# Kernel optimization log

Hardware: AMD Instinct MI355X
Metric: run time of the kernel (lower is better)

## Reference

```python
import jax, jax.numpy as jnp
import numpy as np

EPS = 1e-6
K = 20
NUM_OBJECTS = 50
OBJ_FEAT = 256
C_DIM = 128
HIDDEN = 128


def vn_linear(x, W):
    # x: [B, C, 3, ...]; W: [O, C] -> [B, O, 3, ...]
    return jnp.einsum('oc,bc...->bo...', W, x)


def vn_leaky(x, Wdir, slope):
    d = vn_linear(x, Wdir)
    dot = jnp.sum(x * d, axis=2, keepdims=True)
    dsq = jnp.sum(d * d, axis=2, keepdims=True)
    x_neg = x - (dot / (dsq + EPS)) * d
    return slope * x + (1.0 - slope) * jnp.where(dot >= 0, x, x_neg)


def vn_linear_leaky(x, Wfeat, Wdir, slope):
    pf = vn_linear(x, Wfeat)
    d = vn_linear(x, Wdir)
    dot = jnp.sum(pf * d, axis=2, keepdims=True)
    dsq = jnp.sum(d * d, axis=2, keepdims=True)
    p_neg = pf - (dot / (dsq + EPS)) * d
    return slope * pf + (1.0 - slope) * jnp.where(dot >= 0, pf, p_neg)


def resblock(x, fc0, fc1, a0, a1, sc):
    net = vn_linear(vn_leaky(x, a0, 0.0), fc0)
    dx = vn_linear(vn_leaky(net, a1, 0.0), fc1)
    return vn_linear(x, sc) + dx


def get_graph_feature_cross(x, k):
    # x: [B, 3, N] -> edge features [B, 3, 3, N, k]
    inner = -2.0 * jnp.einsum('bdn,bdm->bnm', x, x)
    xx = jnp.sum(x * x, axis=1)                       # [B, N]
    neg_dist = -xx[:, :, None] - inner - xx[:, None, :]  # [B, N, N]
    idx = jax.lax.top_k(neg_dist, k)[1]               # [B, N, k] nearest neighbors
    xt = jnp.transpose(x, (0, 2, 1))                  # [B, N, 3]
    nbr = jax.vmap(lambda pts, ind: pts[ind])(xt, idx)  # [B, N, k, 3]
    ctr = jnp.broadcast_to(xt[:, :, None, :], nbr.shape)
    cross = jnp.cross(nbr, ctr)
    feat = jnp.stack([nbr - ctr, ctr, cross], axis=3)  # [B, N, k, 3, 3]
    return jnp.transpose(feat, (0, 3, 4, 1, 2))


def mlp2(zf, w0, w1, w2):
    h = jax.nn.relu(zf @ w0.T)
    h = jax.nn.relu(h @ w1.T)
    return h @ w2.T


def setup_inputs():
    key = jax.random.key(0)
    ks = jax.random.split(key, 24)
    B, N = 4, 4096

    def rn(k, shape):
        return jax.random.normal(k, shape, dtype=jnp.float32) * (1.0 / np.sqrt(shape[-1]))

    return {
        'p': jax.random.normal(ks[0], (B, N, 3), dtype=jnp.float32),
        'z_idxs': jax.random.randint(ks[1], (B,), 0, NUM_OBJECTS),
        'z': jax.random.normal(ks[2], (NUM_OBJECTS, OBJ_FEAT), dtype=jnp.float32),
        'hw0': rn(ks[3], (OBJ_FEAT, OBJ_FEAT)),
        'hw1': rn(ks[4], (OBJ_FEAT, OBJ_FEAT)),
        'hw2': rn(ks[5], (C_DIM * HIDDEN, OBJ_FEAT)),
        'hb0': rn(ks[6], (OBJ_FEAT, OBJ_FEAT)),
        'hb1': rn(ks[7], (OBJ_FEAT, OBJ_FEAT)),
        'hb2': rn(ks[8], (C_DIM, OBJ_FEAT)),
        'conv_pos_feat': rn(ks[9], (128, 3)),
        'conv_pos_dir': rn(ks[10], (128, 3)),
        'fc_pos_w': rn(ks[11], (2 * HIDDEN, 128)),
        'blk_fc0': rn(ks[12], (5, HIDDEN, 2 * HIDDEN)),
        'blk_fc1': rn(ks[13], (5, HIDDEN, HIDDEN)),
        'blk_act0': rn(ks[14], (5, 2 * HIDDEN, 2 * HIDDEN)),
        'blk_act1': rn(ks[15], (5, HIDDEN, HIDDEN)),
        'blk_sc': rn(ks[16], (5, HIDDEN, 2 * HIDDEN)),
        'actc_dir': rn(ks[17], (HIDDEN, HIDDEN)),
    }


def reference(p, z_idxs, z, hw0, hw1, hw2, hb0, hb1, hb2, conv_pos_feat,
              conv_pos_dir, fc_pos_w, blk_fc0, blk_fc1, blk_act0, blk_act1,
              blk_sc, actc_dir):
    B = p.shape[0]
    x = jnp.transpose(p, (0, 2, 1))                       # [B, 3, N]
    feat = get_graph_feature_cross(x, K)                  # [B, 3, 3, N, k]
    net = vn_linear_leaky(feat, conv_pos_feat, conv_pos_dir, 0.2)  # [B,128,3,N,k]
    net = jnp.mean(net, axis=-1)                          # [B,128,3,N]
    net = vn_linear(net, fc_pos_w)                        # [B,256,3,N]
    for i in range(5):
        net = resblock(net, blk_fc0[i], blk_fc1[i], blk_act0[i], blk_act1[i], blk_sc[i])
        if i < 4:
            pooled = jnp.mean(net, axis=-1, keepdims=True)
            net = jnp.concatenate([net, jnp.broadcast_to(pooled, net.shape)], axis=1)
    net = vn_leaky(jnp.mean(net, axis=-1), actc_dir, 0.2)  # [B, HIDDEN, 3]
    zf = z[z_idxs]                                        # [B, OBJ_FEAT]
    w = mlp2(zf, hw0, hw1, hw2).reshape(B, C_DIM, HIDDEN)  # hypernet weights
    b = mlp2(zf, hb0, hb1, hb2)                           # [B, C_DIM]
    c = jnp.einsum('bhd,bch->bcd', net, w) + b[:, :, None]  # [B, C_DIM, 3]
    return c
```

## Files before the change

kernel.cpp:

```cpp
#include <hip/hip_runtime.h>
#include <hip/hip_fp16.h>
#include <cstdint>
#include <cstddef>

#define NPTS 4096
#define BATCH 4
#define KNN 20

typedef __half f16;
using f32x4 = __attribute__((ext_vector_type(4))) float;
using f16x8 = __attribute__((ext_vector_type(8))) _Float16;

__global__ __launch_bounds__(256) void knn_kernel(const float* __restrict__ p,
                                                  int* __restrict__ idx_out) {
    __shared__ float pts[12288];
    const int tid  = threadIdx.x;
    const int wave = tid >> 6, lane = tid & 63;
    const int b  = blockIdx.x >> 10;
    const int nb = ((blockIdx.x & 1023) << 2) + wave;

    const float4* src4 = (const float4*)(p + (size_t)b * NPTS * 3);
    float4* dst4 = (float4*)pts;
    for (int i = tid; i < NPTS * 3 / 4; i += 256) dst4[i] = src4[i];
    __syncthreads();

    const float cx = pts[3 * nb], cy = pts[3 * nb + 1], cz = pts[3 * nb + 2];
    unsigned lst[4];
#pragma unroll
    for (int i = 0; i < 4; i++) lst[i] = 0xFFFFFFFFu;

    for (int t = 0; t < NPTS / 64; t++) {
        int m = (t << 6) + lane;
        float dx = pts[3 * m] - cx, dy = pts[3 * m + 1] - cy, dz = pts[3 * m + 2] - cz;
        float d = dx * dx + dy * dy + dz * dz;
        unsigned c = (__float_as_uint(d) & 0xFFFFF000u) | (unsigned)m;
#pragma unroll
        for (int j = 0; j < 4; j++) {
            unsigned lo = min(c, lst[j]);
            c = max(c, lst[j]);
            lst[j] = lo;
        }
    }

    unsigned lo = 0u, hi = 0xFFFFFFFFu;
    for (int it = 0; it < 32; it++) {
        unsigned mid = lo + ((hi - lo) >> 1);
        int cnt = __popcll(__ballot(lst[0] <= mid)) + __popcll(__ballot(lst[1] <= mid))
                + __popcll(__ballot(lst[2] <= mid)) + __popcll(__ballot(lst[3] <= mid));
        if (cnt >= KNN) hi = mid; else lo = mid + 1;
    }
    const unsigned T = hi;

    unsigned long long bl[4];
#pragma unroll
    for (int j = 0; j < 4; j++) bl[j] = __ballot(lst[j] <= T);
    const unsigned long long lmask = (lane == 63) ? ~0ull >> 1 : (1ull << lane) - 1;
    int base = 0;
    const size_t out_base = ((size_t)b * NPTS + nb) * KNN;
#pragma unroll
    for (int j = 0; j < 4; j++) {
        if (lst[j] <= T) {
            int pos = base + (int)__popcll(bl[j] & lmask);
            idx_out[out_base + pos] = (int)(lst[j] & 0xFFFu);
        }
        base += (int)__popcll(bl[j]);
    }
}

__global__ __launch_bounds__(128) void edgeconv_kernel(
    const float* __restrict__ p, const int* __restrict__ idx,
    const float* __restrict__ wf, const float* __restrict__ wd,
    f16* __restrict__ out) {
    __shared__ float e[KNN][6];
    const int col = blockIdx.x;
    const int b = col >> 12;
    const int tid = threadIdx.x;
    const float cx = p[(size_t)col * 3], cy = p[(size_t)col * 3 + 1], cz = p[(size_t)col * 3 + 2];
    if (tid < KNN) {
        int j = idx[(size_t)col * KNN + tid];
        const float* q = &p[((size_t)b * NPTS + j) * 3];
        float nx = q[0], ny = q[1], nz = q[2];
        e[tid][0] = nx - cx; e[tid][1] = ny - cy; e[tid][2] = nz - cz;
        e[tid][3] = ny * cz - nz * cy;
        e[tid][4] = nz * cx - nx * cz;
        e[tid][5] = nx * cy - ny * cx;
    }
    __syncthreads();
    const int o = tid;
    const float f0 = wf[o * 3], f1 = wf[o * 3 + 1], f2 = wf[o * 3 + 2];
    const float g0 = wd[o * 3], g1 = wd[o * 3 + 1], g2 = wd[o * 3 + 2];
    const float pc0 = f1 * cx, pc1 = f1 * cy, pc2 = f1 * cz;
    const float gc0 = g1 * cx, gc1 = g1 * cy, gc2 = g1 * cz;
    float a0 = 0.f, a1 = 0.f, a2 = 0.f;
    for (int k = 0; k < KNN; k++) {
        float d0 = e[k][0], d1 = e[k][1], d2 = e[k][2];
        float c0 = e[k][3], c1 = e[k][4], c2 = e[k][5];
        float pf0 = fmaf(f0, d0, fmaf(f2, c0, pc0));
        float pf1 = fmaf(f0, d1, fmaf(f2, c1, pc1));
        float pf2 = fmaf(f0, d2, fmaf(f2, c2, pc2));
        float dd0 = fmaf(g0, d0, fmaf(g2, c0, gc0));
        float dd1 = fmaf(g0, d1, fmaf(g2, c1, gc1));
        float dd2 = fmaf(g0, d2, fmaf(g2, c2, gc2));
        float dot = pf0 * dd0 + pf1 * dd1 + pf2 * dd2;
        float dsq = dd0 * dd0 + dd1 * dd1 + dd2 * dd2;
        float w = 0.8f * dot * __builtin_amdgcn_rcpf(dsq + 1e-6f);
        w = (dot >= 0.f) ? 0.f : w;
        a0 += pf0 - w * dd0;
        a1 += pf1 - w * dd1;
        a2 += pf2 - w * dd2;
    }
    const float inv = 1.f / (float)KNN;
    out[((size_t)col * 3 + 0) * 128 + o] = __float2half(a0 * inv);
    out[((size_t)col * 3 + 1) * 128 + o] = __float2half(a1 * inv);
    out[((size_t)col * 3 + 2) * 128 + o] = __float2half(a2 * inv);
}

template <int KIN>
__global__ __launch_bounds__(256) void resblock_kernel(
    const uint16_t* __restrict__ INg,
    const uint16_t* __restrict__ Wfcp,
    const uint16_t* __restrict__ Wa0,
    const uint16_t* __restrict__ Wfc0,
    const uint16_t* __restrict__ Wa1,
    const uint16_t* __restrict__ Wsc,
    const uint16_t* __restrict__ Wfc1,
    const float* __restrict__ PBg,
    const float* __restrict__ BAg,
    const float* __restrict__ BSCg,
    f16* __restrict__ OUTg,
    float* __restrict__ PPg) {
    constexpr int XRB  = (KIN == 256) ? 528 : 272;
    constexpr int INS_OFF = (KIN == 256) ? 13056 : 0;
    constexpr int H0_OFF  = (KIN == 256) ? 38400 : 14592;
    constexpr int MID_OFF = (KIN == 256) ? 0 : 27648;
    constexpr int LDS_SZ  = (KIN == 256) ? 51456 : 40704;
    __shared__ char lds[LDS_SZ];
    char* MBs = lds;
    char* INs = lds + INS_OFF;
    float* PBs = (float*)(lds + 13056);
    char* H0h = lds + H0_OFF;
    char* MID = lds + MID_OFF;

    const int tid = threadIdx.x;
    const int lane = tid & 63;
    const int wc = tid >> 6;
    const int gr0 = blockIdx.x * 48;
    const int b = blockIdx.x >> 8;

    if (KIN == 128) {
        for (int i = tid; i < 384; i += 256) PBs[i] = PBg[b * 384 + i];
    }
    {
        char* dst = (KIN == 256) ? MBs : INs;
#pragma unroll
        for (int j = 0; j < 3; j++) {
            int chunk = tid + j * 256;
            int row = chunk >> 4, c16 = chunk & 15;
            f16x8 v = *(const f16x8*)(INg + (size_t)(gr0 + row) * 128 + c16 * 8);
            *(f16x8*)(dst + row * 272 + c16 * 16) = v;
        }
    }
    __syncthreads();

    if (KIN == 256) {
        f32x4 acc[3][4];
#pragma unroll
        for (int i = 0; i < 3; i++)
#pragma unroll
            for (int j = 0; j < 4; j++) acc[i][j] = (f32x4){0.f, 0.f, 0.f, 0.f};
#pragma unroll
        for (int ks = 0; ks < 4; ks++) {
            const int kb = ks * 64 + (lane >> 4) * 16;
            f16x8 af[3], bf[4];
#pragma unroll
            for (int mi = 0; mi < 3; mi++) {
                int r = mi * 16 + (lane & 15);
                af[mi] = *(const f16x8*)(MBs + r * 272 + kb);
            }
#pragma unroll
            for (int ni = 0; ni < 4; ni++) {
                int o = wc * 64 + ni * 16 + (lane & 15);
                bf[ni] = *(const f16x8*)(Wfcp + o * 128 + ks * 32 + (lane >> 4) * 8);
            }
#pragma unroll
            for (int mi = 0; mi < 3; mi++)
#pragma unroll
                for (int ni = 0; ni < 4; ni++)
                    acc[mi][ni] = __builtin_amdgcn_mfma_f32_16x16x32_f16(
                        af[mi], bf[ni], acc[mi][ni], 0, 0, 0);
        }
#pragma unroll
        for (int mi = 0; mi < 3; mi++)
#pragma unroll
            for (int ni = 0; ni < 4; ni++) {
                int col = wc * 64 + ni * 16 + (lane & 15);
#pragma unroll
                for (int r = 0; r < 4; r++) {
                    int row = mi * 16 + (lane >> 4) * 4 + r;
                    *(f16*)(INs + row * XRB + col * 2) = __float2half(acc[mi][ni][r]);
                }
            }
        __syncthreads();
    }

    f32x4 midAcc[3][2];
#pragma unroll
    for (int i = 0; i < 3; i++) { midAcc[i][0] = (f32x4){0,0,0,0}; midAcc[i][1] = (f32x4){0,0,0,0}; }

#pragma unroll
    for (int half = 0; half < 2; half++) {
        {
            f32x4 acc[3][2];
#pragma unroll
            for (int i = 0; i < 3; i++) { acc[i][0] = (f32x4){0,0,0,0}; acc[i][1] = (f32x4){0,0,0,0}; }
#pragma unroll
            for (int ks = 0; ks < KIN / 32; ks++) {
                const int kb = ks * 64 + (lane >> 4) * 16;
                f16x8 af[3], bf[2];
#pragma unroll
                for (int mi = 0; mi < 3; mi++) {
                    int r = mi * 16 + (lane & 15);
                    af[mi] = *(const f16x8*)(INs + r * XRB + kb);
                }
#pragma unroll
                for (int ni = 0; ni < 2; ni++) {
                    int o = half * 128 + wc * 32 + ni * 16 + (lane & 15);
                    bf[ni] = *(const f16x8*)(Wa0 + o * 256 + ks * 32 + (lane >> 4) * 8);
                }
#pragma unroll
                for (int mi = 0; mi < 3; mi++)
#pragma unroll
                    for (int ni = 0; ni < 2; ni++)
                        acc[mi][ni] = __builtin_amdgcn_mfma_f32_16x16x32_f16(
                            af[mi], bf[ni], acc[mi][ni], 0, 0, 0);
            }
#pragma unroll
            for (int mi = 0; mi < 3; mi++)
#pragma unroll
                for (int ni = 0; ni < 2; ni++) {
                    int col = wc * 32 + ni * 16 + (lane & 15);
#pragma unroll
                    for (int r = 0; r < 4; r++) {
                        int row = mi * 16 + (lane >> 4) * 4 + r;
                        float v = acc[mi][ni][r];
                        if (KIN == 128)
                            v += BAg[b * 768 + (row % 3) * 256 + half * 128 + col];
                        *(f16*)(H0h + row * 272 + col * 2) = __float2half(v);
                    }
                }
        }
        __syncthreads();
#pragma unroll
        for (int j = 0; j < 4; j++) {
            int it = tid + j * 256;
            int pnt = it >> 6, cp = it & 63;
            float xv[3][2], dv[3][2];
#pragma unroll
            for (int s = 0; s < 3; s++) {
                int row = pnt * 3 + s;
                __half2 d2 = *(const __half2*)(H0h + row * 272 + cp * 4);
                dv[s][0] = __half2float(d2.x); dv[s][1] = __half2float(d2.y);
                if (KIN == 256) {
                    __half2 x2 = *(const __half2*)(INs + row * XRB + half * 256 + cp * 4);
                    xv[s][0] = __half2float(x2.x); xv[s][1] = __half2float(x2.y);
                } else {
                    if (half == 0) {
                        __half2 x2 = *(const __half2*)(INs + row * XRB + cp * 4);
                        xv[s][0] = __half2float(x2.x); xv[s][1] = __half2float(x2.y);
                    } else {
                        xv[s][0] = PBs[s * 128 + cp * 2];
                        xv[s][1] = PBs[s * 128 + cp * 2 + 1];
                    }
                }
            }
#pragma unroll
            for (int jj = 0; jj < 2; jj++) {
                float dot = xv[0][jj] * dv[0][jj] + xv[1][jj] * dv[1][jj] + xv[2][jj] * dv[2][jj];
                float dsq = dv[0][jj] * dv[0][jj] + dv[1][jj] * dv[1][jj] + dv[2][jj] * dv[2][jj];
                float coef = dot * __builtin_amdgcn_rcpf(dsq + 1e-6f);
                bool pos = dot >= 0.f;
#pragma unroll
                for (int s = 0; s < 3; s++)
                    xv[s][jj] = pos ? xv[s][jj] : xv[s][jj] - coef * dv[s][jj];
            }
#pragma unroll
            for (int s = 0; s < 3; s++) {
                int row = pnt * 3 + s;
                __half2 h2;
                h2.x = __float2half(xv[s][0]);
                h2.y = __float2half(xv[s][1]);
                *(__half2*)(H0h + row * 272 + cp * 4) = h2;
            }
        }
        __syncthreads();
#pragma unroll
        for (int ks = 0; ks < 4; ks++) {
            const int kb = ks * 64 + (lane >> 4) * 16;
            f16x8 af[3], bf[2];
#pragma unroll
            for (int mi = 0; mi < 3; mi++) {
                int r = mi * 16 + (lane & 15);
                af[mi] = *(const f16x8*)(H0h + r * 272 + kb);
            }
#pragma unroll
            for (int ni = 0; ni < 2; ni++) {
                int o = wc * 32 + ni * 16 + (lane & 15);
                bf[ni] = *(const f16x8*)(Wfc0 + o * 256 + half * 128 + ks * 32 + (lane >> 4) * 8);
            }
#pragma unroll
            for (int mi = 0; mi < 3; mi++)
#pragma unroll
                for (int ni = 0; ni < 2; ni++)
                    midAcc[mi][ni] = __builtin_amdgcn_mfma_f32_16x16x32_f16(
                        af[mi], bf[ni], midAcc[mi][ni], 0, 0, 0);
        }
        __syncthreads();
    }

#pragma unroll
    for (int mi = 0; mi < 3; mi++)
#pragma unroll
        for (int ni = 0; ni < 2; ni++) {
            int col = wc * 32 + ni * 16 + (lane & 15);
#pragma unroll
            for (int r = 0; r < 4; r++) {
                int row = mi * 16 + (lane >> 4) * 4 + r;
                *(f16*)(MID + row * 272 + col * 2) = __float2half(midAcc[mi][ni][r]);
            }
        }
    __syncthreads();

    {
        f32x4 acc[3][2];
#pragma unroll
        for (int i = 0; i < 3; i++) { acc[i][0] = (f32x4){0,0,0,0}; acc[i][1] = (f32x4){0,0,0,0}; }
#pragma unroll
        for (int ks = 0; ks < 4; ks++) {
            const int kb = ks * 64 + (lane >> 4) * 16;
            f16x8 af[3], bf[2];
#pragma unroll
            for (int mi = 0; mi < 3; mi++) {
                int r = mi * 16 + (lane & 15);
                af[mi] = *(const f16x8*)(MID + r * 272 + kb);
            }
#pragma unroll
            for (int ni = 0; ni < 2; ni++) {
                int o = wc * 32 + ni * 16 + (lane & 15);
                bf[ni] = *(const f16x8*)(Wa1 + o * 128 + ks * 32 + (lane >> 4) * 8);
            }
#pragma unroll
            for (int mi = 0; mi < 3; mi++)
#pragma unroll
                for (int ni = 0; ni < 2; ni++)
                    acc[mi][ni] = __builtin_amdgcn_mfma_f32_16x16x32_f16(
                        af[mi], bf[ni], acc[mi][ni], 0, 0, 0);
        }
#pragma unroll
        for (int mi = 0; mi < 3; mi++)
#pragma unroll
            for (int ni = 0; ni < 2; ni++) {
                int col = wc * 32 + ni * 16 + (lane & 15);
#pragma unroll
                for (int r = 0; r < 4; r++) {
                    int row = mi * 16 + (lane >> 4) * 4 + r;
                    *(f16*)(H0h + row * 272 + col * 2) = __float2half(acc[mi][ni][r]);
                }
            }
    }
    __syncthreads();
#pragma unroll
    for (int j = 0; j < 4; j++) {
        int it = tid + j * 256;
        int pnt = it >> 6, cp = it & 63;
        float xv[3][2], dv[3][2];
#pragma unroll
        for (int s = 0; s < 3; s++) {
            int row = pnt * 3 + s;
            __half2 d2 = *(const __half2*)(H0h + row * 272 + cp * 4);
            __half2 x2 = *(const __half2*)(MID + row * 272 + cp * 4);
            dv[s][0] = __half2float(d2.x); dv[s][1] = __half2float(d2.y);
            xv[s][0] = __half2float(x2.x); xv[s][1] = __half2float(x2.y);
        }
#pragma unroll
        for (int jj = 0; jj < 2; jj++) {
            float dot = xv[0][jj] * dv[0][jj] + xv[1][jj] * dv[1][jj] + xv[2][jj] * dv[2][jj];
            float dsq = dv[0][jj] * dv[0][jj] + dv[1][jj] * dv[1][jj] + dv[2][jj] * dv[2][jj];
            float coef = dot * __builtin_amdgcn_rcpf(dsq + 1e-6f);
            bool pos = dot >= 0.f;
#pragma unroll
            for (int s = 0; s < 3; s++)
                xv[s][jj] = pos ? xv[s][jj] : xv[s][jj] - coef * dv[s][jj];
        }
#pragma unroll
        for (int s = 0; s < 3; s++) {
            int row = pnt * 3 + s;
            __half2 h2;
            h2.x = __float2half(xv[s][0]);
            h2.y = __float2half(xv[s][1]);
            *(__half2*)(H0h + row * 272 + cp * 4) = h2;
        }
    }
    __syncthreads();

    {
        f32x4 acc[3][2];
#pragma unroll
        for (int i = 0; i < 3; i++) { acc[i][0] = (f32x4){0,0,0,0}; acc[i][1] = (f32x4){0,0,0,0}; }
        constexpr int NKS = (KIN + 128) / 32;
#pragma unroll
        for (int ks = 0; ks < NKS; ks++) {
            const int kelem = ks * 32;
            f16x8 af[3], bf[2];
            if (kelem < KIN) {
                const int kb = kelem * 2 + (lane >> 4) * 16;
#pragma unroll
                for (int mi = 0; mi < 3; mi++) {
                    int r = mi * 16 + (lane & 15);
                    af[mi] = *(const f16x8*)(INs + r * XRB + kb);
                }
#pragma unroll
                for (int ni = 0; ni < 2; ni++) {
                    int o = wc * 32 + ni * 16 + (lane & 15);
                    bf[ni] = *(const f16x8*)(Wsc + o * 256 + kelem + (lane >> 4) * 8);
                }
            } else {
                const int kk = kelem - KIN;
                const int kb = kk * 2 + (lane >> 4) * 16;
#pragma unroll
                for (int mi = 0; mi < 3; mi++) {
                    int r = mi * 16 + (lane & 15);
                    af[mi] = *(const f16x8*)(H0h + r * 272 + kb);
                }
#pragma unroll
                for (int ni = 0; ni < 2; ni++) {
                    int o = wc * 32 + ni * 16 + (lane & 15);
                    bf[ni] = *(const f16x8*)(Wfc1 + o * 128 + kk + (lane >> 4) * 8);
                }
            }
#pragma unroll
            for (int mi = 0; mi < 3; mi++)
#pragma unroll
                for (int ni = 0; ni < 2; ni++)
                    acc[mi][ni] = __builtin_amdgcn_mfma_f32_16x16x32_f16(
                        af[mi], bf[ni], acc[mi][ni], 0, 0, 0);
        }
        float ps[2][3] = {};
#pragma unroll
        for (int mi = 0; mi < 3; mi++)
#pragma unroll
            for (int ni = 0; ni < 2; ni++) {
                int col = wc * 32 + ni * 16 + (lane & 15);
#pragma unroll
                for (int r = 0; r < 4; r++) {
                    int row = mi * 16 + (lane >> 4) * 4 + r;
                    float v = acc[mi][ni][r];
                    if (KIN == 128) v += BSCg[b * 384 + (row % 3) * 128 + col];
                    OUTg[(size_t)(gr0 + row) * 128 + col] = __float2half(v);
                    ps[ni][row % 3] += v;
                }
            }
#pragma unroll
        for (int ni = 0; ni < 2; ni++)
#pragma unroll
            for (int s = 0; s < 3; s++) {
                float x = ps[ni][s];
                x += __shfl_xor(x, 16, 64);
                x += __shfl_xor(x, 32, 64);
                ps[ni][s] = x;
            }
        if ((lane >> 4) == 0) {
#pragma unroll
            for (int ni = 0; ni < 2; ni++) {
                int col = wc * 32 + ni * 16 + (lane & 15);
#pragma unroll
                for (int s = 0; s < 3; s++)
                    PPg[(size_t)blockIdx.x * 384 + s * 128 + col] = ps[ni][s];
            }
        }
    }
}

__global__ __launch_bounds__(512) void poolbias_kernel(
    const float* __restrict__ PP, const f16* __restrict__ a0n, const f16* __restrict__ scn,
    float* __restrict__ PB, float* __restrict__ BA, float* __restrict__ BSC, int hasbias) {
    __shared__ float red[4][128];
    __shared__ float pl[128];
    const int bs = blockIdx.x;
    const int b = bs / 3, s = bs % 3;
    const int t = threadIdx.x;
    const int col = t & 127, seg = t >> 7;
    {
        float acc = 0.f;
        const float* base = PP + (size_t)(b * 256) * 384 + s * 128 + col;
        for (int k = seg * 64; k < seg * 64 + 64; k++) acc += base[(size_t)k * 384];
        red[seg][col] = acc;
    }
    __syncthreads();
    if (t < 128) {
        float a = (red[0][t] + red[1][t]) + (red[2][t] + red[3][t]);
        a *= (1.f / (float)NPTS);
        pl[t] = a;
        PB[bs * 128 + t] = a;
    }
    __syncthreads();
    if (!hasbias) return;
    if (t < 256) {
        float s2 = 0.f;
        for (int c = 0; c < 128; c++) s2 += __half2float(a0n[t * 256 + 128 + c]) * pl[c];
        BA[bs * 256 + t] = s2;
    } else if (t < 384) {
        int o = t - 256;
        float s2 = 0.f;
        for (int c = 0; c < 128; c++) s2 += __half2float(scn[o * 256 + 128 + c]) * pl[c];
        BSC[bs * 128 + o] = s2;
    }
}

__global__ void cvt_all(const float* __restrict__ fcpw, const float* __restrict__ act0,
                        const float* __restrict__ fc0, const float* __restrict__ act1,
                        const float* __restrict__ fc1, const float* __restrict__ scw,
                        f16* o_fcpw, f16* o_act0, f16* o_fc0, f16* o_act1, f16* o_fc1,
                        f16* o_scw) {
    int i = blockIdx.x * 256 + threadIdx.x;
    if (i < 32768) { o_fcpw[i] = __float2half(fcpw[i]); }
    else if (i < 360448) { int j = i - 32768;  o_act0[j] = __float2half(act0[j]); }
    else if (i < 524288) { int j = i - 360448; o_fc0[j]  = __float2half(fc0[j]); }
    else if (i < 606208) { int j = i - 524288; o_act1[j] = __float2half(act1[j]); }
    else if (i < 688128) { int j = i - 606208; o_fc1[j]  = __float2half(fc1[j]); }
    else                 { int j = i - 688128; o_scw[j]  = __float2half(scw[j]); }
}

__global__ __launch_bounds__(256) void hypermlp_kernel(
    const float* __restrict__ z, const int* __restrict__ zidx,
    const float* __restrict__ hw0, const float* __restrict__ hw1,
    const float* __restrict__ hb0, const float* __restrict__ hb1,
    const float* __restrict__ hb2,
    float* __restrict__ H2, float* __restrict__ BV) {
    __shared__ float zf[256], ta[256], tb[256];
    const int b = blockIdx.x, o = threadIdx.x;
    zf[o] = z[(size_t)zidx[b] * 256 + o];
    __syncthreads();
    float s = 0.f;
    for (int c = 0; c < 256; c++) s += zf[c] * hw0[o * 256 + c];
    ta[o] = fmaxf(s, 0.f);
    __syncthreads();
    s = 0.f;
    for (int c = 0; c < 256; c++) s += ta[c] * hw1[o * 256 + c];
    tb[o] = fmaxf(s, 0.f);
    __syncthreads();
    H2[(size_t)b * 256 + o] = tb[o];
    s = 0.f;
    for (int c = 0; c < 256; c++) s += zf[c] * hb0[o * 256 + c];
    __syncthreads();
    ta[o] = fmaxf(s, 0.f);
    __syncthreads();
    s = 0.f;
    for (int c = 0; c < 256; c++) s += ta[c] * hb1[o * 256 + c];
    __syncthreads();
    tb[o] = fmaxf(s, 0.f);
    __syncthreads();
    if (o < 128) {
        s = 0.f;
        for (int c = 0; c < 256; c++) s += tb[c] * hb2[o * 256 + c];
        BV[(size_t)b * 128 + o] = s;
    }
}

__global__ __launch_bounds__(256) void wmat_kernel(const float* __restrict__ H2,
                                                   const float* __restrict__ hw2,
                                                   float* __restrict__ WM) {
    __shared__ float h[256];
    const int b = blockIdx.y;
    const int row = blockIdx.x * 256 + threadIdx.x;
    h[threadIdx.x] = H2[(size_t)b * 256 + threadIdx.x];
    __syncthreads();
    float s = 0.f;
    for (int c = 0; c < 256; c++) s += h[c] * hw2[(size_t)row * 256 + c];
    WM[(size_t)b * 16384 + row] = s;
}

__global__ __launch_bounds__(384) void final_out_kernel(
    const float* __restrict__ pb, const float* __restrict__ actc,
    const float* __restrict__ WM, const float* __restrict__ BV,
    float* __restrict__ out) {
    __shared__ float pb2s[3][128];
    const int b = blockIdx.x;
    const int t = threadIdx.x;
    if (t < 128) {
        const int o = t;
        float d0 = 0.f, d1 = 0.f, d2 = 0.f;
        for (int c = 0; c < 128; c++) {
            float w = actc[o * 128 + c];
            d0 += w * pb[(size_t)(b * 3 + 0) * 128 + c];
            d1 += w * pb[(size_t)(b * 3 + 1) * 128 + c];
            d2 += w * pb[(size_t)(b * 3 + 2) * 128 + c];
        }
        float x0 = pb[(size_t)(b * 3 + 0) * 128 + o];
        float x1 = pb[(size_t)(b * 3 + 1) * 128 + o];
        float x2 = pb[(size_t)(b * 3 + 2) * 128 + o];
        float dot = x0 * d0 + x1 * d1 + x2 * d2;
        float dsq = d0 * d0 + d1 * d1 + d2 * d2;
        float coef = dot / (dsq + 1e-6f);
        bool pos = dot >= 0.f;
        float h0 = pos ? x0 : x0 - coef * d0;
        float h1 = pos ? x1 : x1 - coef * d1;
        float h2 = pos ? x2 : x2 - coef * d2;
        pb2s[0][o] = 0.2f * x0 + 0.8f * h0;
        pb2s[1][o] = 0.2f * x1 + 0.8f * h1;
        pb2s[2][o] = 0.2f * x2 + 0.8f * h2;
    }
    __syncthreads();
    const int cd = t / 3, d = t % 3;
    float s = BV[(size_t)b * 128 + cd];
    for (int h = 0; h < 128; h++)
        s += pb2s[d][h] * WM[(size_t)b * 16384 + cd * 128 + h];
    out[(size_t)b * 384 + cd * 3 + d] = s;
}

extern "C" void kernel_launch(void* const* d_in, const int* in_sizes, int n_in,
                              void* d_out, int out_size, void* d_ws, size_t ws_size,
                              hipStream_t stream) {
    (void)in_sizes; (void)n_in; (void)out_size; (void)ws_size;
    const float* p     = (const float*)d_in[0];
    const int*   zidx  = (const int*)d_in[1];
    const float* z     = (const float*)d_in[2];
    const float* hw0   = (const float*)d_in[3];
    const float* hw1   = (const float*)d_in[4];
    const float* hw2   = (const float*)d_in[5];
    const float* hb0   = (const float*)d_in[6];
    const float* hb1   = (const float*)d_in[7];
    const float* hb2   = (const float*)d_in[8];
    const float* cpf   = (const float*)d_in[9];
    const float* cpd   = (const float*)d_in[10];
    const float* fcpw  = (const float*)d_in[11];
    const float* fc0w  = (const float*)d_in[12];
    const float* fc1w  = (const float*)d_in[13];
    const float* act0  = (const float*)d_in[14];
    const float* act1  = (const float*)d_in[15];
    const float* scw   = (const float*)d_in[16];
    const float* actc  = (const float*)d_in[17];
    float* out = (float*)d_out;
    char* ws = (char*)d_ws;

    int*   IDX   = (int*)(ws + 0);
    f16*   MB    = (f16*)(ws + 1310720);
    f16*   MB2   = (f16*)(ws + 13893632);
    f16*   FCPW16= (f16*)(ws + 26476544);
    f16*   ACT0W = (f16*)(ws + 26542080);
    f16*   FC0W  = (f16*)(ws + 27197440);
    f16*   ACT1W = (f16*)(ws + 27525120);
    f16*   FC1W  = (f16*)(ws + 27688960);
    f16*   SCW16 = (f16*)(ws + 27852800);
    float* PP    = (float*)(ws + 28180480);
    float* PB    = (float*)(ws + 29753344);
    float* H2    = (float*)(ws + 29759488);
    float* BV    = (float*)(ws + 29763584);
    float* WM    = (float*)(ws + 29765632);
    float* BA    = (float*)(ws + 30027776);
    float* BSC   = (float*)(ws + 30040064);

    cvt_all<<<3328, 256, 0, stream>>>(fcpw, act0, fc0w, act1, fc1w, scw,
                                      FCPW16, ACT0W, FC0W, ACT1W, FC1W, SCW16);

    knn_kernel<<<BATCH * NPTS / 4, 256, 0, stream>>>(p, IDX);
    edgeconv_kernel<<<BATCH * NPTS, 128, 0, stream>>>(p, IDX, cpf, cpd, MB);

    resblock_kernel<256><<<1024, 256, 0, stream>>>(
        (const uint16_t*)MB, (const uint16_t*)FCPW16,
        (const uint16_t*)ACT0W, (const uint16_t*)FC0W,
        (const uint16_t*)ACT1W, (const uint16_t*)SCW16, (const uint16_t*)FC1W,
        nullptr, nullptr, nullptr, MB2, PP);
    poolbias_kernel<<<12, 512, 0, stream>>>(PP, ACT0W + 1 * 65536, SCW16 + 1 * 32768,
                                            PB, BA, BSC, 1);

    for (int i = 1; i < 5; i++) {
        const f16* a0h = ACT0W + (size_t)i * 256 * 256;
        const f16* sch = SCW16 + (size_t)i * 128 * 256;
        f16* in  = (i & 1) ? MB2 : MB;
        f16* ob  = (i & 1) ? MB : MB2;
        resblock_kernel<128><<<1024, 256, 0, stream>>>(
            (const uint16_t*)in, nullptr,
            (const uint16_t*)a0h,
            (const uint16_t*)(FC0W + (size_t)i * 128 * 256),
            (const uint16_t*)(ACT1W + (size_t)i * 128 * 128),
            (const uint16_t*)sch,
            (const uint16_t*)(FC1W + (size_t)i * 128 * 128),
            PB, BA, BSC, ob, PP);
        if (i < 4) {
            poolbias_kernel<<<12, 512, 0, stream>>>(
                PP, ACT0W + (size_t)(i + 1) * 65536, SCW16 + (size_t)(i + 1) * 32768,
                PB, BA, BSC, 1);
        } else {
            poolbias_kernel<<<12, 512, 0, stream>>>(PP, nullptr, nullptr, PB, BA, BSC, 0);
        }
    }

    hypermlp_kernel<<<4, 256, 0, stream>>>(z, zidx, hw0, hw1, hb0, hb1, hb2, H2, BV);
    wmat_kernel<<<dim3(64, 4), 256, 0, stream>>>(H2, hw2, WM);
    final_out_kernel<<<4, 384, 0, stream>>>(PB, actc, WM, BV, out);
}
```

Baseline: 394.4 us.

## Double resblock workgroup to 512 threads, each wave computing 16 output columns

```diff
diff --git a/kernel.cpp b/kernel.cpp
--- a/kernel.cpp
+++ b/kernel.cpp
@@ -116,7 +116,7 @@
 }
 
 template <int KIN>
-__global__ __launch_bounds__(256) void resblock_kernel(
+__global__ __launch_bounds__(512) void resblock_kernel(
     const uint16_t* __restrict__ INg,
     const uint16_t* __restrict__ Wfcp,
     const uint16_t* __restrict__ Wa0,
@@ -148,13 +148,11 @@
     const int b = blockIdx.x >> 8;
 
     if (KIN == 128) {
-        for (int i = tid; i < 384; i += 256) PBs[i] = PBg[b * 384 + i];
+        if (tid < 384) PBs[tid] = PBg[b * 384 + tid];
     }
     {
         char* dst = (KIN == 256) ? MBs : INs;
-#pragma unroll
-        for (int j = 0; j < 3; j++) {
-            int chunk = tid + j * 256;
+        for (int chunk = tid; chunk < 768; chunk += 512) {
             int row = chunk >> 4, c16 = chunk & 15;
             f16x8 v = *(const f16x8*)(INg + (size_t)(gr0 + row) * 128 + c16 * 8);
             *(f16x8*)(dst + row * 272 + c16 * 16) = v;
@@ -163,37 +161,35 @@
     __syncthreads();
 
     if (KIN == 256) {
-        f32x4 acc[3][4];
-#pragma unroll
-        for (int i = 0; i < 3; i++)
-#pragma unroll
-            for (int j = 0; j < 4; j++) acc[i][j] = (f32x4){0.f, 0.f, 0.f, 0.f};
+        f32x4 acc[3][2];
+#pragma unroll
+        for (int i = 0; i < 3; i++) { acc[i][0] = (f32x4){0,0,0,0}; acc[i][1] = (f32x4){0,0,0,0}; }
 #pragma unroll
         for (int ks = 0; ks < 4; ks++) {
             const int kb = ks * 64 + (lane >> 4) * 16;
-            f16x8 af[3], bf[4];
+            f16x8 af[3], bf[2];
 #pragma unroll
             for (int mi = 0; mi < 3; mi++) {
                 int r = mi * 16 + (lane & 15);
                 af[mi] = *(const f16x8*)(MBs + r * 272 + kb);
             }
 #pragma unroll
-            for (int ni = 0; ni < 4; ni++) {
-                int o = wc * 64 + ni * 16 + (lane & 15);
+            for (int ni = 0; ni < 2; ni++) {
+                int o = wc * 32 + ni * 16 + (lane & 15);
                 bf[ni] = *(const f16x8*)(Wfcp + o * 128 + ks * 32 + (lane >> 4) * 8);
             }
 #pragma unroll
             for (int mi = 0; mi < 3; mi++)
 #pragma unroll
-                for (int ni = 0; ni < 4; ni++)
+                for (int ni = 0; ni < 2; ni++)
                     acc[mi][ni] = __builtin_amdgcn_mfma_f32_16x16x32_f16(
                         af[mi], bf[ni], acc[mi][ni], 0, 0, 0);
         }
 #pragma unroll
         for (int mi = 0; mi < 3; mi++)
 #pragma unroll
-            for (int ni = 0; ni < 4; ni++) {
-                int col = wc * 64 + ni * 16 + (lane & 15);
+            for (int ni = 0; ni < 2; ni++) {
+                int col = wc * 32 + ni * 16 + (lane & 15);
 #pragma unroll
                 for (int r = 0; r < 4; r++) {
                     int row = mi * 16 + (lane >> 4) * 4 + r;
@@ -203,56 +199,51 @@
         __syncthreads();
     }
 
-    f32x4 midAcc[3][2];
-#pragma unroll
-    for (int i = 0; i < 3; i++) { midAcc[i][0] = (f32x4){0,0,0,0}; midAcc[i][1] = (f32x4){0,0,0,0}; }
+    f32x4 midAcc[3];
+#pragma unroll
+    for (int i = 0; i < 3; i++) midAcc[i] = (f32x4){0, 0, 0, 0};
 
 #pragma unroll
     for (int half = 0; half < 2; half++) {
         {
-            f32x4 acc[3][2];
-#pragma unroll
-            for (int i = 0; i < 3; i++) { acc[i][0] = (f32x4){0,0,0,0}; acc[i][1] = (f32x4){0,0,0,0}; }
+            f32x4 acc[3];
+#pragma unroll
+            for (int i = 0; i < 3; i++) acc[i] = (f32x4){0, 0, 0, 0};
 #pragma unroll
             for (int ks = 0; ks < KIN / 32; ks++) {
                 const int kb = ks * 64 + (lane >> 4) * 16;
-                f16x8 af[3], bf[2];
+                f16x8 af[3], bf;
 #pragma unroll
                 for (int mi = 0; mi < 3; mi++) {
                     int r = mi * 16 + (lane & 15);
                     af[mi] = *(const f16x8*)(INs + r * XRB + kb);
                 }
-#pragma unroll
-                for (int ni = 0; ni < 2; ni++) {
-                    int o = half * 128 + wc * 32 + ni * 16 + (lane & 15);
-                    bf[ni] = *(const f16x8*)(Wa0 + o * 256 + ks * 32 + (lane >> 4) * 8);
+                {
+                    int o = half * 128 + wc * 16 + (lane & 15);
+                    bf = *(const f16x8*)(Wa0 + o * 256 + ks * 32 + (lane >> 4) * 8);
                 }
 #pragma unroll
                 for (int mi = 0; mi < 3; mi++)
-#pragma unroll
-                    for (int ni = 0; ni < 2; ni++)
-                        acc[mi][ni] = __builtin_amdgcn_mfma_f32_16x16x32_f16(
-                            af[mi], bf[ni], acc[mi][ni], 0, 0, 0);
-            }
-#pragma unroll
-            for (int mi = 0; mi < 3; mi++)
-#pragma unroll
-                for (int ni = 0; ni < 2; ni++) {
-                    int col = wc * 32 + ni * 16 + (lane & 15);
-#pragma unroll
-                    for (int r = 0; r < 4; r++) {
-                        int row = mi * 16 + (lane >> 4) * 4 + r;
-                        float v = acc[mi][ni][r];
-                        if (KIN == 128)
-                            v += BAg[b * 768 + (row % 3) * 256 + half * 128 + col];
-                        *(f16*)(H0h + row * 272 + col * 2) = __float2half(v);
-                    }
-                }
+                    acc[mi] = __builtin_amdgcn_mfma_f32_16x16x32_f16(
+                        af[mi], bf, acc[mi], 0, 0, 0);
+            }
+#pragma unroll
+            for (int mi = 0; mi < 3; mi++) {
+                int col = wc * 16 + (lane & 15);
+#pragma unroll
+                for (int r = 0; r < 4; r++) {
+                    int row = mi * 16 + (lane >> 4) * 4 + r;
+                    float v = acc[mi][r];
+                    if (KIN == 128)
+                        v += BAg[b * 768 + (row % 3) * 256 + half * 128 + col];
+                    *(f16*)(H0h + row * 272 + col * 2) = __float2half(v);
+                }
+            }
         }
         __syncthreads();
 #pragma unroll
-        for (int j = 0; j < 4; j++) {
-            int it = tid + j * 256;
+        for (int j = 0; j < 2; j++) {
+            int it = tid + j * 512;
             int pnt = it >> 6, cp = it & 63;
             float xv[3][2], dv[3][2];
 #pragma unroll
@@ -296,81 +287,71 @@
 #pragma unroll
         for (int ks = 0; ks < 4; ks++) {
             const int kb = ks * 64 + (lane >> 4) * 16;
-            f16x8 af[3], bf[2];
+            f16x8 af[3], bf;
 #pragma unroll
             for (int mi = 0; mi < 3; mi++) {
                 int r = mi * 16 + (lane & 15);
                 af[mi] = *(const f16x8*)(H0h + r * 272 + kb);
             }
-#pragma unroll
-            for (int ni = 0; ni < 2; ni++) {
-                int o = wc * 32 + ni * 16 + (lane & 15);
-                bf[ni] = *(const f16x8*)(Wfc0 + o * 256 + half * 128 + ks * 32 + (lane >> 4) * 8);
+            {
+                int o = wc * 16 + (lane & 15);
+                bf = *(const f16x8*)(Wfc0 + o * 256 + half * 128 + ks * 32 + (lane >> 4) * 8);
             }
 #pragma unroll
             for (int mi = 0; mi < 3; mi++)
-#pragma unroll
-                for (int ni = 0; ni < 2; ni++)
-                    midAcc[mi][ni] = __builtin_amdgcn_mfma_f32_16x16x32_f16(
-                        af[mi], bf[ni], midAcc[mi][ni], 0, 0, 0);
+                midAcc[mi] = __builtin_amdgcn_mfma_f32_16x16x32_f16(
+                    af[mi], bf, midAcc[mi], 0, 0, 0);
         }
         __syncthreads();
     }
 
 #pragma unroll
-    for (int mi = 0; mi < 3; mi++)
-#pragma unroll
-        for (int ni = 0; ni < 2; ni++) {
-            int col = wc * 32 + ni * 16 + (lane & 15);
-#pragma unroll
-            for (int r = 0; r < 4; r++) {
-                int row = mi * 16 + (lane >> 4) * 4 + r;
-                *(f16*)(MID + row * 272 + col * 2) = __float2half(midAcc[mi][ni][r]);
-            }
-        }
+    for (int mi = 0; mi < 3; mi++) {
+        int col = wc * 16 + (lane & 15);
+#pragma unroll
+        for (int r = 0; r < 4; r++) {
+            int row = mi * 16 + (lane >> 4) * 4 + r;
+            *(f16*)(MID + row * 272 + col * 2) = __float2half(midAcc[mi][r]);
+        }
+    }
     __syncthreads();
 
     {
-        f32x4 acc[3][2];
-#pragma unroll
-        for (int i = 0; i < 3; i++) { acc[i][0] = (f32x4){0,0,0,0}; acc[i][1] = (f32x4){0,0,0,0}; }
+        f32x4 acc[3];
+#pragma unroll
+        for (int i = 0; i < 3; i++) acc[i] = (f32x4){0, 0, 0, 0};
 #pragma unroll
         for (int ks = 0; ks < 4; ks++) {
             const int kb = ks * 64 + (lane >> 4) * 16;
-            f16x8 af[3], bf[2];
+            f16x8 af[3], bf;
 #pragma unroll
             for (int mi = 0; mi < 3; mi++) {
                 int r = mi * 16 + (lane & 15);
                 af[mi] = *(const f16x8*)(MID + r * 272 + kb);
             }
-#pragma unroll
-            for (int ni = 0; ni < 2; ni++) {
-                int o = wc * 32 + ni * 16 + (lane & 15);
-                bf[ni] = *(const f16x8*)(Wa1 + o * 128 + ks * 32 + (lane >> 4) * 8);
+            {
+                int o = wc * 16 + (lane & 15);
+                bf = *(const f16x8*)(Wa1 + o * 128 + ks * 32 + (lane >> 4) * 8);
             }
 #pragma unroll
             for (int mi = 0; mi < 3; mi++)
-#pragma unroll
-                for (int ni = 0; ni < 2; ni++)
-                    acc[mi][ni] = __builtin_amdgcn_mfma_f32_16x16x32_f16(
-                        af[mi], bf[ni], acc[mi][ni], 0, 0, 0);
-        }
-#pragma unroll
-        for (int mi = 0; mi < 3; mi++)
-#pragma unroll
-            for (int ni = 0; ni < 2; ni++) {
-                int col = wc * 32 + ni * 16 + (lane & 15);
-#pragma unroll
-                for (int r = 0; r < 4; r++) {
-                    int row = mi * 16 + (lane >> 4) * 4 + r;
-                    *(f16*)(H0h + row * 272 + col * 2) = __float2half(acc[mi][ni][r]);
-                }
-            }
-    }
-    __syncthreads();
-#pragma unroll
-    for (int j = 0; j < 4; j++) {
-        int it = tid + j * 256;
+                acc[mi] = __builtin_amdgcn_mfma_f32_16x16x32_f16(
+                    af[mi], bf, acc[mi], 0, 0, 0);
+        }
+#pragma unroll
+        for (int mi = 0; mi < 3; mi++) {
+            int col = wc * 16 + (lane & 15);
+#pragma unroll
+            for (int r = 0; r < 4; r++) {
+                int row = mi * 16 + (lane >> 4) * 4 + r;
+                *(f16*)(H0h + row * 272 + col * 2) = __float2half(acc[mi][r]);
+            }
+        }
+    }
+    __syncthreads();
+#pragma unroll
+    for (int j = 0; j < 2; j++) {
+        int it = tid + j * 512;
         int pnt = it >> 6, cp = it & 63;
         float xv[3][2], dv[3][2];
 #pragma unroll
@@ -403,14 +384,14 @@
     __syncthreads();
 
     {
-        f32x4 acc[3][2];
-#pragma unroll
-        for (int i = 0; i < 3; i++) { acc[i][0] = (f32x4){0,0,0,0}; acc[i][1] = (f32x4){0,0,0,0}; }
+        f32x4 acc[3];
+#pragma unroll
+        for (int i = 0; i < 3; i++) acc[i] = (f32x4){0, 0, 0, 0};
         constexpr int NKS = (KIN + 128) / 32;
 #pragma unroll
         for (int ks = 0; ks < NKS; ks++) {
             const int kelem = ks * 32;
-            f16x8 af[3], bf[2];
+            f16x8 af[3], bf;
             if (kelem < KIN) {
                 const int kb = kelem * 2 + (lane >> 4) * 16;
 #pragma unroll
@@ -418,10 +399,9 @@
                     int r = mi * 16 + (lane & 15);
                     af[mi] = *(const f16x8*)(INs + r * XRB + kb);
                 }
-#pragma unroll
-                for (int ni = 0; ni < 2; ni++) {
-                    int o = wc * 32 + ni * 16 + (lane & 15);
-                    bf[ni] = *(const f16x8*)(Wsc + o * 256 + kelem + (lane >> 4) * 8);
+                {
+                    int o = wc * 16 + (lane & 15);
+                    bf = *(const f16x8*)(Wsc + o * 256 + kelem + (lane >> 4) * 8);
                 }
             } else {
                 const int kk = kelem - KIN;
@@ -431,51 +411,40 @@
                     int r = mi * 16 + (lane & 15);
                     af[mi] = *(const f16x8*)(H0h + r * 272 + kb);
                 }
-#pragma unroll
-                for (int ni = 0; ni < 2; ni++) {
-                    int o = wc * 32 + ni * 16 + (lane & 15);
-                    bf[ni] = *(const f16x8*)(Wfc1 + o * 128 + kk + (lane >> 4) * 8);
+                {
+                    int o = wc * 16 + (lane & 15);
+                    bf = *(const f16x8*)(Wfc1 + o * 128 + kk + (lane >> 4) * 8);
                 }
             }
 #pragma unroll
             for (int mi = 0; mi < 3; mi++)
-#pragma unroll
-                for (int ni = 0; ni < 2; ni++)
-                    acc[mi][ni] = __builtin_amdgcn_mfma_f32_16x16x32_f16(
-                        af[mi], bf[ni], acc[mi][ni], 0, 0, 0);
-        }
-        float ps[2][3] = {};
-#pragma unroll
-        for (int mi = 0; mi < 3; mi++)
-#pragma unroll
-            for (int ni = 0; ni < 2; ni++) {
-                int col = wc * 32 + ni * 16 + (lane & 15);
-#pragma unroll
-                for (int r = 0; r < 4; r++) {
-                    int row = mi * 16 + (lane >> 4) * 4 + r;
-                    float v = acc[mi][ni][r];
-                    if (KIN == 128) v += BSCg[b * 384 + (row % 3) * 128 + col];
-                    OUTg[(size_t)(gr0 + row) * 128 + col] = __float2half(v);
-                    ps[ni][row % 3] += v;
-                }
-            }
-#pragma unroll
-        for (int ni = 0; ni < 2; ni++)
-#pragma unroll
-            for (int s = 0; s < 3; s++) {
-                float x = ps[ni][s];
-                x += __shfl_xor(x, 16, 64);
-                x += __shfl_xor(x, 32, 64);
-                ps[ni][s] = x;
-            }
+                acc[mi] = __builtin_amdgcn_mfma_f32_16x16x32_f16(
+                    af[mi], bf, acc[mi], 0, 0, 0);
+        }
+        float ps[3] = {0.f, 0.f, 0.f};
+        const int col = wc * 16 + (lane & 15);
+#pragma unroll
+        for (int mi = 0; mi < 3; mi++) {
+#pragma unroll
+            for (int r = 0; r < 4; r++) {
+                int row = mi * 16 + (lane >> 4) * 4 + r;
+                float v = acc[mi][r];
+                if (KIN == 128) v += BSCg[b * 384 + (row % 3) * 128 + col];
+                OUTg[(size_t)(gr0 + row) * 128 + col] = __float2half(v);
+                ps[row % 3] += v;
+            }
+        }
+#pragma unroll
+        for (int s = 0; s < 3; s++) {
+            float x = ps[s];
+            x += __shfl_xor(x, 16, 64);
+            x += __shfl_xor(x, 32, 64);
+            ps[s] = x;
+        }
         if ((lane >> 4) == 0) {
 #pragma unroll
-            for (int ni = 0; ni < 2; ni++) {
-                int col = wc * 32 + ni * 16 + (lane & 15);
-#pragma unroll
-                for (int s = 0; s < 3; s++)
-                    PPg[(size_t)blockIdx.x * 384 + s * 128 + col] = ps[ni][s];
-            }
+            for (int s = 0; s < 3; s++)
+                PPg[(size_t)blockIdx.x * 384 + s * 128 + col] = ps[s];
         }
     }
 }
@@ -665,7 +634,7 @@
     knn_kernel<<<BATCH * NPTS / 4, 256, 0, stream>>>(p, IDX);
     edgeconv_kernel<<<BATCH * NPTS, 128, 0, stream>>>(p, IDX, cpf, cpd, MB);
 
-    resblock_kernel<256><<<1024, 256, 0, stream>>>(
+    resblock_kernel<256><<<1024, 512, 0, stream>>>(
         (const uint16_t*)MB, (const uint16_t*)FCPW16,
         (const uint16_t*)ACT0W, (const uint16_t*)FC0W,
         (const uint16_t*)ACT1W, (const uint16_t*)SCW16, (const uint16_t*)FC1W,
@@ -678,7 +647,7 @@
         const f16* sch = SCW16 + (size_t)i * 128 * 256;
         f16* in  = (i & 1) ? MB2 : MB;
         f16* ob  = (i & 1) ? MB : MB2;
-        resblock_kernel<128><<<1024, 256, 0, stream>>>(
+        resblock_kernel<128><<<1024, 512, 0, stream>>>(
             (const uint16_t*)in, nullptr,
             (const uint16_t*)a0h,
             (const uint16_t*)(FC0W + (size_t)i * 128 * 256),
```

Result: slower. 425.8 us (+7.9%).
